# Kernel tuning notes

Hardware: AMD Instinct MI355X
Metric: run time of the kernel (lower is better)

## Reference

```python
import jax, jax.numpy as jnp
import numpy as np

N_NODES = 50000
N_EDGES = 1000000
IN_CH = 256
HID_CH = 128
HEADS = 2
OUT_CH = 3
NEG_SLOPE = 0.2  # PyG GATConv default leaky_relu slope


def setup_inputs() -> dict:
    key = jax.random.key(0)
    ks = jax.random.split(key, 10)
    s = 0.1
    x = jax.random.normal(ks[0], (N_NODES, IN_CH), dtype=jnp.float32)
    edge_index = jax.random.randint(ks[1], (2, N_EDGES), 0, N_NODES, dtype=jnp.int64)
    # GATConv layer 1 (heads=2, concat=True)
    W1 = jax.random.normal(ks[2], (IN_CH, HEADS * HID_CH), dtype=jnp.float32) * s
    a_src1 = jax.random.normal(ks[3], (HEADS, HID_CH), dtype=jnp.float32) * s
    a_dst1 = jax.random.normal(ks[4], (HEADS, HID_CH), dtype=jnp.float32) * s
    b1 = jnp.zeros((HEADS * HID_CH,), dtype=jnp.float32)
    # GATConv layer 2 (heads=1, concat=False)
    W2 = jax.random.normal(ks[5], (HEADS * HID_CH, OUT_CH), dtype=jnp.float32) * s
    a_src2 = jax.random.normal(ks[6], (1, OUT_CH), dtype=jnp.float32) * s
    a_dst2 = jax.random.normal(ks[7], (1, OUT_CH), dtype=jnp.float32) * s
    b2 = jnp.zeros((OUT_CH,), dtype=jnp.float32)
    return dict(x=x, edge_index=edge_index, W1=W1, a_src1=a_src1, a_dst1=a_dst1,
                b1=b1, W2=W2, a_src2=a_src2, a_dst2=a_dst2, b2=b2)


def gat_layer(x, edge_index, W, a_src, a_dst, b, concat):
    # x: [N, F_in]; W: [F_in, H*C]; a_src/a_dst: [H, C]
    n = x.shape[0]
    H, C = a_src.shape
    h = (x @ W).reshape(n, H, C)                       # [N, H, C]
    al_s = jnp.einsum('nhc,hc->nh', h, a_src)          # [N, H]
    al_d = jnp.einsum('nhc,hc->nh', h, a_dst)          # [N, H]
    src, dst = edge_index[0], edge_index[1]
    e = jax.nn.leaky_relu(al_s[src] + al_d[dst], NEG_SLOPE)   # [E, H]
    # segment softmax over incoming edges of each dst node
    e_max = jax.ops.segment_max(e, dst, num_segments=n)       # [N, H]
    w = jnp.exp(e - e_max[dst])                                # [E, H]
    denom = jax.ops.segment_sum(w, dst, num_segments=n)        # [N, H]
    alpha = w / jnp.maximum(denom[dst], 1e-16)                 # [E, H]
    out = jax.ops.segment_sum(h[src] * alpha[:, :, None], dst, num_segments=n)  # [N, H, C]
    out = out.reshape(n, H * C) if concat else out.mean(axis=1)
    return out + b


def reference(x, edge_index, W1, a_src1, a_dst1, b1, W2, a_src2, a_dst2, b2):
    # dropout(p=0.6) is identity in eval mode
    h = jax.nn.elu(gat_layer(x, edge_index, W1, a_src1, a_dst1, b1, concat=True))
    h = gat_layer(h, edge_index, W2, a_src2, a_dst2, b2, concat=False)
    return jax.nn.log_softmax(h, axis=1)
```

## Files before the change

### kernel.cpp

```cpp
#include <hip/hip_runtime.h>

#define N_NODES 50000
#define N_EDGES 1000000
#define FIN 256
#define F1  256
#define OUTC 3
#define SUBCAP 32
#define GEMM_BLOCKS ((N_NODES + 63) / 64)
#define EDGE_BLOCKS ((N_EDGES + 255) / 256)
#define NODE_BLOCKS ((N_NODES + 3) / 4)
#define AGG_NB (N_NODES / 16)

typedef __attribute__((ext_vector_type(8))) short  short8;
typedef __attribute__((ext_vector_type(4))) float  f32x4;
typedef __attribute__((ext_vector_type(2))) float  f32x2;
typedef __attribute__((ext_vector_type(4))) _Float16 h16x4;

__device__ __forceinline__ unsigned short f2bf(float f) {
  unsigned int x; __builtin_memcpy(&x, &f, 4);
  x += 0x7fffu + ((x >> 16) & 1u);
  return (unsigned short)(x >> 16);
}
__device__ __forceinline__ float u2f(unsigned int x) {
  float f; __builtin_memcpy(&f, &x, 4); return f;
}
__device__ __forceinline__ float wredmax(float v) {
  #pragma unroll
  for (int m = 32; m > 0; m >>= 1) v = fmaxf(v, __shfl_xor(v, m));
  return v;
}
__device__ __forceinline__ float wredsum(float v) {
  #pragma unroll
  for (int m = 32; m > 0; m >>= 1) v += __shfl_xor(v, m);
  return v;
}

__global__ __launch_bounds__(256) void k_t(const float* __restrict__ w1,
                                           unsigned short* __restrict__ w1t,
                                           int* __restrict__ deg2) {
  int idx = blockIdx.x * 256 + threadIdx.x;
  int k = idx >> 8, n = idx & 255;
  w1t[n * 256 + k] = f2bf(w1[k * 256 + n]);
  if (idx < 2 * N_NODES) deg2[idx] = 0;
  int i2 = idx + 65536;
  if (i2 < 2 * N_NODES) deg2[i2] = 0;
}

__global__ __launch_bounds__(256) void k_bg(
    const float* __restrict__ x,
    const unsigned short* __restrict__ w1t,
    const float* __restrict__ a_src1,
    const float* __restrict__ a_dst1,
    unsigned short* __restrict__ h1b,
    float* __restrict__ als1,
    float* __restrict__ ald1,
    const int* __restrict__ ei,
    int* __restrict__ deg2, unsigned short* __restrict__ bucket) {
  const int t = threadIdx.x;

  if (blockIdx.x >= GEMM_BLOCKS) {
    __shared__ int sflag;
    if (t < 64) {
      int idx = 2 * (t * 15625 + 7) + 1;
      unsigned long long b = __ballot(ei[idx] != 0);
      if (t == 0) sflag = (b != 0ull) ? 1 : 0;
    }
    __syncthreads();
    const int f = sflag;
    int e = (blockIdx.x - GEMM_BLOCKS) * 256 + t;
    if (e < N_EDGES) {
      int s, d;
      if (f) { s = ei[e];     d = ei[N_EDGES + e]; }
      else   { s = ei[2 * e]; d = ei[2 * (N_EDGES + e)]; }
      int sub = e & 1;
      int pos = atomicAdd(&deg2[d * 2 + sub], 1);
      if (pos < SUBCAP) bucket[d * 64 + sub * SUBCAP + pos] = (unsigned short)s;
    }
    return;
  }

  const int wv   = t >> 6;
  const int lane = t & 63;
  const int m    = lane & 15;
  const int quad = lane >> 4;
  const int row0 = blockIdx.x * 64 + wv * 16;

  int arow = row0 + m;
  if (arow > N_NODES - 1) arow = N_NODES - 1;
  const float* xrow = x + (size_t)arow * FIN + quad * 8;

  short8 af[8];
  #pragma unroll
  for (int kk = 0; kk < 8; ++kk) {
    f32x4 v0 = *(const f32x4*)(xrow + kk * 32);
    f32x4 v1 = *(const f32x4*)(xrow + kk * 32 + 4);
    short8 fr;
    #pragma unroll
    for (int j = 0; j < 4; ++j) {
      fr[j]     = (short)f2bf(v0[j]);
      fr[j + 4] = (short)f2bf(v1[j]);
    }
    af[kk] = fr;
  }

  f32x4 acc[16];
  #pragma unroll
  for (int c = 0; c < 16; ++c) {
    const unsigned short* bp = w1t + (size_t)(c * 16 + m) * FIN + quad * 8;
    f32x4 a = {0.f, 0.f, 0.f, 0.f};
    #pragma unroll
    for (int kk = 0; kk < 8; ++kk) {
      short8 bf = *(const short8*)(bp + kk * 32);
      a = __builtin_amdgcn_mfma_f32_16x16x32_bf16(af[kk], bf, a, 0, 0, 0);
    }
    acc[c] = a;
  }

  float s0[4] = {0,0,0,0}, s1[4] = {0,0,0,0}, d0[4] = {0,0,0,0}, d1[4] = {0,0,0,0};
  #pragma unroll
  for (int c = 0; c < 16; ++c) {
    int ch = c * 16 + m;
    float av = a_src1[ch];
    float dv = a_dst1[ch];
    if (c < 8) {
      #pragma unroll
      for (int r = 0; r < 4; ++r) { s0[r] += acc[c][r] * av; d0[r] += acc[c][r] * dv; }
    } else {
      #pragma unroll
      for (int r = 0; r < 4; ++r) { s1[r] += acc[c][r] * av; d1[r] += acc[c][r] * dv; }
    }
  }
  #pragma unroll
  for (int msk = 1; msk < 16; msk <<= 1) {
    #pragma unroll
    for (int r = 0; r < 4; ++r) {
      s0[r] += __shfl_xor(s0[r], msk);
      s1[r] += __shfl_xor(s1[r], msk);
      d0[r] += __shfl_xor(d0[r], msk);
      d1[r] += __shfl_xor(d1[r], msk);
    }
  }
  #pragma unroll
  for (int r = 0; r < 4; ++r) {
    int row = row0 + quad * 4 + r;
    if (row < N_NODES) {
      unsigned short* hrow = h1b + (size_t)row * F1 + m;
      #pragma unroll
      for (int c = 0; c < 16; ++c) hrow[c * 16] = f2bf(acc[c][r]);
      if (m == 0) {
        als1[row * 2 + 0] = s0[r]; als1[row * 2 + 1] = s1[r];
        ald1[row * 2 + 0] = d0[r]; ald1[row * 2 + 1] = d1[r];
      }
    }
  }
}

__global__ __launch_bounds__(256) void k_alpha(
    const unsigned short* __restrict__ bucket,
    const int* __restrict__ deg2,
    const float* __restrict__ als1,
    const float* __restrict__ ald1,
    unsigned int* __restrict__ pack0,
    unsigned int* __restrict__ pack1) {
  const int wv   = threadIdx.x >> 6;
  const int lane = threadIdx.x & 63;
  const int n = blockIdx.x * 4 + wv;
  if (n >= N_NODES) return;
  const int c0 = min(deg2[n * 2 + 0], SUBCAP);
  const int c1 = min(deg2[n * 2 + 1], SUBCAP);
  const int dg = c0 + c1;
  const float ad0  = ald1[n * 2 + 0];
  const float ad1v = ald1[n * 2 + 1];
  const float2* alsv = (const float2*)als1;

  float l0 = -1e30f, l1 = -1e30f; int s = 0;
  if (lane < dg) {
    int bidx = lane < c0 ? lane : (SUBCAP + lane - c0);
    s = (int)bucket[n * 64 + bidx];
    float2 a = alsv[s];
    l0 = a.x + ad0;  l0 = l0 > 0.f ? l0 : 0.2f * l0;
    l1 = a.y + ad1v; l1 = l1 > 0.f ? l1 : 0.2f * l1;
  }
  const float m0 = wredmax(l0), m1 = wredmax(l1);
  const float e0 = (lane < dg) ? __expf(l0 - m0) : 0.f;
  const float e1 = (lane < dg) ? __expf(l1 - m1) : 0.f;
  const float sum0 = wredsum(e0), sum1 = wredsum(e1);
  unsigned int q0 = (unsigned int)rintf(e0 / fmaxf(sum0, 1e-16f) * 65535.f);
  unsigned int q1 = (unsigned int)rintf(e1 / fmaxf(sum1, 1e-16f) * 65535.f);
  unsigned int su = (unsigned int)s << 16;
  pack0[n * 64 + lane] = su | q0;
  pack1[n * 64 + lane] = su | q1;
}

__global__ __launch_bounds__(256) void k_agg(
    const int* __restrict__ deg2,
    const unsigned int* __restrict__ pack0,
    const unsigned int* __restrict__ pack1,
    const unsigned int* __restrict__ h1b32,
    unsigned int* __restrict__ h2agg32) {
  const int chunk = blockIdx.x & 7;
  const int nb    = blockIdx.x >> 3;
  const int g     = threadIdx.x >> 4;
  const int l16   = threadIdx.x & 15;
  const int n = nb * 16 + g;

  const int c0 = min(deg2[n * 2 + 0], SUBCAP);
  const int c1 = min(deg2[n * 2 + 1], SUBCAP);
  const int dg = c0 + c1;

  const unsigned int* pk = (chunk >= 4 ? pack1 : pack0) + (size_t)n * 64;
  unsigned int r0 = __builtin_nontemporal_load(pk + l16);
  unsigned int r1 = (dg > 16) ? __builtin_nontemporal_load(pk + 16 + l16) : 0u;
  unsigned int r2 = (dg > 32) ? __builtin_nontemporal_load(pk + 32 + l16) : 0u;
  unsigned int r3 = (dg > 48) ? __builtin_nontemporal_load(pk + 48 + l16) : 0u;

  const unsigned int* slab = h1b32 + chunk * 16 + l16;
  f32x2 acc = {0.f, 0.f};

  #define AGG_ROUND(RQ, BASE)                                              \
    if (BASE < dg) {                                                       \
      _Pragma("unroll")                                                    \
      for (int j = 0; j < 16; ++j) {                                       \
        unsigned int rec = (unsigned int)__shfl((int)(RQ), j, 16);         \
        float a = (float)(rec & 0xffffu) * (1.f / 65535.f);                \
        unsigned int u = slab[(size_t)(rec >> 16) * 128];                  \
        f32x2 h; h.x = u2f(u << 16); h.y = u2f(u & 0xffff0000u);           \
        f32x2 av = {a, a};                                                 \
        acc = __builtin_elementwise_fma(av, h, acc);                       \
      }                                                                    \
    }
  AGG_ROUND(r0, 0)
  AGG_ROUND(r1, 16)
  AGG_ROUND(r2, 32)
  AGG_ROUND(r3, 48)
  #undef AGG_ROUND

  _Float16 o0 = (_Float16)acc.x, o1 = (_Float16)acc.y;
  unsigned short w0, w1;
  __builtin_memcpy(&w0, &o0, 2);
  __builtin_memcpy(&w1, &o1, 2);
  unsigned int ow = (unsigned int)w0 | ((unsigned int)w1 << 16);
  __builtin_nontemporal_store(ow, h2agg32 + (size_t)n * 128 + chunk * 16 + l16);
}

__global__ __launch_bounds__(256) void k_post(
    const _Float16* __restrict__ h2agg,
    const float* __restrict__ b1,
    const float* __restrict__ w2,
    const float* __restrict__ a_src2,
    const float* __restrict__ a_dst2,
    float4* __restrict__ h2pack,
    float* __restrict__ ald2) {
  const int wv   = threadIdx.x >> 6;
  const int lane = threadIdx.x & 63;
  const int n = blockIdx.x * 4 + wv;
  if (n >= N_NODES) return;
  h16x4 hv = *(const h16x4*)(h2agg + (size_t)n * F1 + lane * 4);
  float p0 = 0.f, p1 = 0.f, p2 = 0.f;
  #pragma unroll
  for (int j = 0; j < 4; ++j) {
    int ch = lane * 4 + j;
    float tt = (float)hv[j] + b1[ch];
    tt = tt > 0.f ? tt : __expf(tt) - 1.f;
    p0 = fmaf(tt, w2[ch * 3 + 0], p0);
    p1 = fmaf(tt, w2[ch * 3 + 1], p1);
    p2 = fmaf(tt, w2[ch * 3 + 2], p2);
  }
  p0 = wredsum(p0);
  p1 = wredsum(p1);
  p2 = wredsum(p2);
  if (lane == 0) {
    float als2v = p0 * a_src2[0] + p1 * a_src2[1] + p2 * a_src2[2];
    h2pack[n] = make_float4(p0, p1, p2, als2v);
    ald2[n] = p0 * a_dst2[0] + p1 * a_dst2[1] + p2 * a_dst2[2];
  }
}

__global__ __launch_bounds__(256) void k_attn2(
    const unsigned short* __restrict__ bucket,
    const int* __restrict__ deg2,
    const float4* __restrict__ h2pack,
    const float* __restrict__ ald2,
    const float* __restrict__ b2,
    float* __restrict__ out) {
  const int wv   = threadIdx.x >> 6;
  const int lane = threadIdx.x & 63;
  const int n = blockIdx.x * 4 + wv;
  if (n >= N_NODES) return;
  const int c0 = min(deg2[n * 2 + 0], SUBCAP);
  const int c1 = min(deg2[n * 2 + 1], SUBCAP);
  const int dg = c0 + c1;
  const float adn = ald2[n];

  float l = -1e30f;
  float4 hp = make_float4(0.f, 0.f, 0.f, 0.f);
  if (lane < dg) {
    int bidx = lane < c0 ? lane : (SUBCAP + lane - c0);
    int s = (int)bucket[n * 64 + bidx];
    hp = h2pack[s];
    l = hp.w + adn;
    l = l > 0.f ? l : 0.2f * l;
  }
  const float m = wredmax(l);
  const float e = (lane < dg) ? __expf(l - m) : 0.f;
  const float sum = wredsum(e);
  const float inv = 1.f / fmaxf(sum, 1e-16f);
  float p0 = wredsum(e * hp.x);
  float p1 = wredsum(e * hp.y);
  float p2 = wredsum(e * hp.z);

  if (lane == 0) {
    float o0 = p0 * inv + b2[0];
    float o1 = p1 * inv + b2[1];
    float o2 = p2 * inv + b2[2];
    float mm = fmaxf(o0, fmaxf(o1, o2));
    float ls = logf(__expf(o0 - mm) + __expf(o1 - mm) + __expf(o2 - mm));
    out[n * 3 + 0] = o0 - mm - ls;
    out[n * 3 + 1] = o1 - mm - ls;
    out[n * 3 + 2] = o2 - mm - ls;
  }
}

extern "C" void kernel_launch(void* const* d_in, const int* in_sizes, int n_in,
                              void* d_out, int out_size, void* d_ws, size_t ws_size,
                              hipStream_t stream) {
  (void)in_sizes; (void)n_in; (void)out_size; (void)ws_size;
  const float* x      = (const float*)d_in[0];
  const int*   ei     = (const int*)d_in[1];
  const float* W1     = (const float*)d_in[2];
  const float* a_src1 = (const float*)d_in[3];
  const float* a_dst1 = (const float*)d_in[4];
  const float* b1     = (const float*)d_in[5];
  const float* W2     = (const float*)d_in[6];
  const float* a_src2 = (const float*)d_in[7];
  const float* a_dst2 = (const float*)d_in[8];
  const float* b2     = (const float*)d_in[9];
  float* out = (float*)d_out;

  char* p = (char*)d_ws;
  auto alloc = [&](size_t bytes) -> char* {
    char* r = p; p += (bytes + 511) & ~(size_t)511; return r;
  };
  unsigned short* w1t  = (unsigned short*)alloc(65536ull * 2);
  unsigned short* h1b  = (unsigned short*)alloc((size_t)N_NODES * F1 * 2);
  float*  als1   = (float*)alloc((size_t)N_NODES * 2 * 4);
  float*  ald1   = (float*)alloc((size_t)N_NODES * 2 * 4);
  float4* h2pack = (float4*)alloc((size_t)N_NODES * 16);
  float*  ald2   = (float*)alloc((size_t)N_NODES * 4);
  int*    deg2   = (int*)alloc((size_t)N_NODES * 2 * 4);
  unsigned short* bucket = (unsigned short*)alloc((size_t)N_NODES * 64 * 2);
  unsigned int* pack0 = (unsigned int*)alloc((size_t)N_NODES * 64 * 4);
  unsigned int* pack1 = (unsigned int*)alloc((size_t)N_NODES * 64 * 4);
  unsigned int* h2agg32 = (unsigned int*)alloc((size_t)N_NODES * 128 * 4);

  hipLaunchKernelGGL(k_t, dim3(256), dim3(256), 0, stream, W1, w1t, deg2);
  hipLaunchKernelGGL(k_bg, dim3(GEMM_BLOCKS + EDGE_BLOCKS), dim3(256), 0, stream,
                     x, w1t, a_src1, a_dst1, h1b, als1, ald1, ei, deg2, bucket);
  hipLaunchKernelGGL(k_alpha, dim3(NODE_BLOCKS), dim3(256), 0, stream,
                     bucket, deg2, als1, ald1, pack0, pack1);
  hipLaunchKernelGGL(k_agg, dim3(8 * AGG_NB), dim3(256), 0, stream,
                     deg2, pack0, pack1, (const unsigned int*)h1b, h2agg32);
  hipLaunchKernelGGL(k_post, dim3(NODE_BLOCKS), dim3(256), 0, stream,
                     (const _Float16*)h2agg32, b1, W2, a_src2, a_dst2, h2pack, ald2);
  hipLaunchKernelGGL(k_attn2, dim3(NODE_BLOCKS), dim3(256), 0, stream,
                     bucket, deg2, h2pack, ald2, b2, out);
}
```

Before: 302.9 us.

## Store h1 in per-chunk planes and simplify aggregation loop to direct pack reads

The GEMM now writes h1 in a chunked planar layout (8 planes of 32 bf16 per node), so each aggregation chunk gathers from a compact 64-byte-per-node plane instead of strided 512-byte rows, which is meant to improve cache locality for the random gathers. The aggregation loop replaces the shuffle-broadcast rounds with a plain loop over the degree that reads pack records directly (uniform across the 16-lane group). k_alpha now skips writing pack entries beyond the node degree, cutting write traffic. The direct pack reads add one load per edge per lane, served from cache as broadcasts.

```diff
diff --git a/kernel.cpp b/kernel.cpp
--- a/kernel.cpp
+++ b/kernel.cpp
@@ -51,7 +51,7 @@
     const unsigned short* __restrict__ w1t,
     const float* __restrict__ a_src1,
     const float* __restrict__ a_dst1,
-    unsigned short* __restrict__ h1b,
+    unsigned short* __restrict__ h1c,
     float* __restrict__ als1,
     float* __restrict__ ald1,
     const int* __restrict__ ei,
@@ -144,9 +144,12 @@
   for (int r = 0; r < 4; ++r) {
     int row = row0 + quad * 4 + r;
     if (row < N_NODES) {
-      unsigned short* hrow = h1b + (size_t)row * F1 + m;
       #pragma unroll
-      for (int c = 0; c < 16; ++c) hrow[c * 16] = f2bf(acc[c][r]);
+      for (int c = 0; c < 16; ++c) {
+        size_t addr = (size_t)(c >> 1) * ((size_t)N_NODES * 32)
+                    + (size_t)row * 32 + (c & 1) * 16 + m;
+        h1c[addr] = f2bf(acc[c][r]);
+      }
       if (m == 0) {
         als1[row * 2 + 0] = s0[r]; als1[row * 2 + 1] = s1[r];
         ald1[row * 2 + 0] = d0[r]; ald1[row * 2 + 1] = d1[r];
@@ -185,18 +188,20 @@
   const float e0 = (lane < dg) ? __expf(l0 - m0) : 0.f;
   const float e1 = (lane < dg) ? __expf(l1 - m1) : 0.f;
   const float sum0 = wredsum(e0), sum1 = wredsum(e1);
-  unsigned int q0 = (unsigned int)rintf(e0 / fmaxf(sum0, 1e-16f) * 65535.f);
-  unsigned int q1 = (unsigned int)rintf(e1 / fmaxf(sum1, 1e-16f) * 65535.f);
-  unsigned int su = (unsigned int)s << 16;
-  pack0[n * 64 + lane] = su | q0;
-  pack1[n * 64 + lane] = su | q1;
+  if (lane < dg) {
+    unsigned int q0 = (unsigned int)rintf(e0 / fmaxf(sum0, 1e-16f) * 65535.f);
+    unsigned int q1 = (unsigned int)rintf(e1 / fmaxf(sum1, 1e-16f) * 65535.f);
+    unsigned int su = (unsigned int)s << 16;
+    pack0[n * 64 + lane] = su | q0;
+    pack1[n * 64 + lane] = su | q1;
+  }
 }
 
 __global__ __launch_bounds__(256) void k_agg(
     const int* __restrict__ deg2,
     const unsigned int* __restrict__ pack0,
     const unsigned int* __restrict__ pack1,
-    const unsigned int* __restrict__ h1b32,
+    const unsigned int* __restrict__ h1c32,
     unsigned int* __restrict__ h2agg32) {
   const int chunk = blockIdx.x & 7;
   const int nb    = blockIdx.x >> 3;
@@ -209,31 +214,18 @@
   const int dg = c0 + c1;
 
   const unsigned int* pk = (chunk >= 4 ? pack1 : pack0) + (size_t)n * 64;
-  unsigned int r0 = __builtin_nontemporal_load(pk + l16);
-  unsigned int r1 = (dg > 16) ? __builtin_nontemporal_load(pk + 16 + l16) : 0u;
-  unsigned int r2 = (dg > 32) ? __builtin_nontemporal_load(pk + 32 + l16) : 0u;
-  unsigned int r3 = (dg > 48) ? __builtin_nontemporal_load(pk + 48 + l16) : 0u;
-
-  const unsigned int* slab = h1b32 + chunk * 16 + l16;
+  const unsigned int* plane = h1c32 + (size_t)chunk * ((size_t)N_NODES * 16) + l16;
+
   f32x2 acc = {0.f, 0.f};
-
-  #define AGG_ROUND(RQ, BASE)                                              \
-    if (BASE < dg) {                                                       \
-      _Pragma("unroll")                                                    \
-      for (int j = 0; j < 16; ++j) {                                       \
-        unsigned int rec = (unsigned int)__shfl((int)(RQ), j, 16);         \
-        float a = (float)(rec & 0xffffu) * (1.f / 65535.f);                \
-        unsigned int u = slab[(size_t)(rec >> 16) * 128];                  \
-        f32x2 h; h.x = u2f(u << 16); h.y = u2f(u & 0xffff0000u);           \
-        f32x2 av = {a, a};                                                 \
-        acc = __builtin_elementwise_fma(av, h, acc);                       \
-      }                                                                    \
-    }
-  AGG_ROUND(r0, 0)
-  AGG_ROUND(r1, 16)
-  AGG_ROUND(r2, 32)
-  AGG_ROUND(r3, 48)
-  #undef AGG_ROUND
+  #pragma unroll 4
+  for (int j = 0; j < dg; ++j) {
+    unsigned int rec = pk[j];
+    float a = (float)(rec & 0xffffu) * (1.f / 65535.f);
+    unsigned int u = plane[(size_t)(rec >> 16) * 16];
+    f32x2 h; h.x = u2f(u << 16); h.y = u2f(u & 0xffff0000u);
+    f32x2 av = {a, a};
+    acc = __builtin_elementwise_fma(av, h, acc);
+  }
 
   _Float16 o0 = (_Float16)acc.x, o1 = (_Float16)acc.y;
   unsigned short w0, w1;
@@ -342,7 +334,7 @@
     char* r = p; p += (bytes + 511) & ~(size_t)511; return r;
   };
   unsigned short* w1t  = (unsigned short*)alloc(65536ull * 2);
-  unsigned short* h1b  = (unsigned short*)alloc((size_t)N_NODES * F1 * 2);
+  unsigned short* h1c  = (unsigned short*)alloc((size_t)N_NODES * F1 * 2);
   float*  als1   = (float*)alloc((size_t)N_NODES * 2 * 4);
   float*  ald1   = (float*)alloc((size_t)N_NODES * 2 * 4);
   float4* h2pack = (float4*)alloc((size_t)N_NODES * 16);
@@ -355,11 +347,11 @@
 
   hipLaunchKernelGGL(k_t, dim3(256), dim3(256), 0, stream, W1, w1t, deg2);
   hipLaunchKernelGGL(k_bg, dim3(GEMM_BLOCKS + EDGE_BLOCKS), dim3(256), 0, stream,
-                     x, w1t, a_src1, a_dst1, h1b, als1, ald1, ei, deg2, bucket);
+                     x, w1t, a_src1, a_dst1, h1c, als1, ald1, ei, deg2, bucket);
   hipLaunchKernelGGL(k_alpha, dim3(NODE_BLOCKS), dim3(256), 0, stream,
                      bucket, deg2, als1, ald1, pack0, pack1);
   hipLaunchKernelGGL(k_agg, dim3(8 * AGG_NB), dim3(256), 0, stream,
-                     deg2, pack0, pack1, (const unsigned int*)h1b, h2agg32);
+                     deg2, pack0, pack1, (const unsigned int*)h1c, h2agg32);
   hipLaunchKernelGGL(k_post, dim3(NODE_BLOCKS), dim3(256), 0, stream,
                      (const _Float16*)h2agg32, b1, W2, a_src2, a_dst2, h2pack, ald2);
   hipLaunchKernelGGL(k_attn2, dim3(NODE_BLOCKS), dim3(256), 0, stream,
```

New measurement: 292.7 us. -3.4%, faster.
